# Performance work log

Measured on AMD Instinct MI355X. Metric: run time of the kernel, lower is better.

Reference implementation:

```python
import jax, jax.numpy as jnp
import numpy as np

B, S, D = 4, 2048, 1024

def setup_inputs() -> dict:
    key = jax.random.key(0)
    k1, k2, k3, k4 = jax.random.split(key, 4)
    scale = 1.0 / np.sqrt(D)
    x = jax.random.normal(k1, (B, S, D), dtype=jnp.float32)
    Wq = jax.random.normal(k2, (D, D), dtype=jnp.float32) * scale
    Wk = jax.random.normal(k3, (D, D), dtype=jnp.float32) * scale
    Wv = jax.random.normal(k4, (D, D), dtype=jnp.float32) * scale
    return {"x": x, "Wq": Wq, "Wk": Wk, "Wv": Wv}

def reference(x, Wq, Wk, Wv):
    # Linear projections (nn.Linear with bias=False computes x @ W.T)
    q = jnp.einsum('bsd,ed->bse', x, Wq)
    k = jnp.einsum('bsd,ed->bse', x, Wk)
    v = jnp.einsum('bsd,ed->bse', x, Wv)
    # HRR binding: circular convolution of k and v == elementwise product in FFT domain
    fq = jnp.fft.fft(q, axis=-1)
    fk = jnp.fft.fft(k, axis=-1)
    fv = jnp.fft.fft(v, axis=-1)
    # Causal associative memory: cumulative sum of bound key-value pairs over sequence
    mem = jnp.cumsum(fk * fv, axis=-2)  # [B, S, D] complex
    # Unbind with query via approximate inverse (complex conjugate of fft(q))
    out = jnp.fft.ifft(mem * jnp.conj(fq), axis=-1).real
    return out.astype(x.dtype)
```

## Files before the change

### kernel.cpp

```cpp
#include <hip/hip_runtime.h>

#define BB 4
#define SS 2048
#define DD 1024
#define MM 8192
#define CH 64
#define RR 32
#define PI_F 3.14159265358979323846f

typedef __attribute__((ext_vector_type(8))) short bf16x8;
typedef __attribute__((ext_vector_type(4))) float f32x4;

__device__ __forceinline__ unsigned short f2bf(float f) {
  unsigned int u = __float_as_uint(f);
  u = (u + 0x7FFFu + ((u >> 16) & 1u)) >> 16;
  return (unsigned short)u;
}
__device__ __forceinline__ float bf2f(unsigned short h) {
  return __uint_as_float(((unsigned int)h) << 16);
}

__global__ __launch_bounds__(256) void convert_bf16(
    const float* __restrict__ src, unsigned short* __restrict__ dst) {
  const long i = ((long)blockIdx.x * 256 + threadIdx.x) * 4;
  const float4 v = *(const float4*)&src[i];
  ushort4 o;
  o.x = f2bf(v.x); o.y = f2bf(v.y); o.z = f2bf(v.z); o.w = f2bf(v.w);
  *(ushort4*)&dst[i] = o;
}

__global__ __launch_bounds__(256) void convert_w(
    const float* __restrict__ Wq, const float* __restrict__ Wk,
    const float* __restrict__ Wv, unsigned short* __restrict__ dst) {
  const int z = blockIdx.y;
  const float* src = (z == 0) ? Wq : (z == 1) ? Wk : Wv;
  const long i = ((long)blockIdx.x * 256 + threadIdx.x) * 4;
  const float4 v = *(const float4*)&src[i];
  ushort4 o;
  o.x = f2bf(v.x); o.y = f2bf(v.y); o.z = f2bf(v.z); o.w = f2bf(v.w);
  *(ushort4*)&dst[(size_t)z * DD * DD + i] = o;
}

__device__ __forceinline__ void async16(const void* g, void* l) {
  __builtin_amdgcn_global_load_lds(
      (const __attribute__((address_space(1))) void*)g,
      (__attribute__((address_space(3))) void*)l, 16, 0, 0);
}

__global__ __launch_bounds__(256) void gemm_mfma(
    const unsigned short* __restrict__ xb,
    const unsigned short* __restrict__ Wb,
    float* __restrict__ outq, unsigned short* __restrict__ KV) {
  const int z = blockIdx.z;
  const unsigned short* W = Wb + (size_t)z * DD * DD;

  __shared__ unsigned short Als[128 * 64];
  __shared__ unsigned short Bls[128 * 64];

  const int tid  = threadIdx.x;
  const int lane = tid & 63;
  const int wave = tid >> 6;
  const int wm = (wave & 1) * 64;
  const int wn = (wave >> 1) * 64;

  const long m0 = (long)blockIdx.x * 128;
  const long n0 = (long)blockIdx.y * 128;

  f32x4 acc[4][4] = {};

  for (int k0 = 0; k0 < DD; k0 += 64) {
    #pragma unroll
    for (int i = 0; i < 4; ++i) {
      const int slot = i * 256 + tid;
      const int row  = slot >> 3;
      const int kq   = slot & 7;
      const int g    = kq ^ (row & 7);
      async16(xb + (m0 + row) * DD + k0 + g * 8, &Als[slot * 8]);
      async16(W  + (n0 + row) * DD + k0 + g * 8, &Bls[slot * 8]);
    }
    __syncthreads();

    const int fr = lane & 15;
    const int kq = lane >> 4;
    #pragma unroll
    for (int h = 0; h < 2; ++h) {
      bf16x8 af[4], bfr[4];
      #pragma unroll
      for (int mt = 0; mt < 4; ++mt) {
        const int row = wm + mt * 16 + fr;
        af[mt] = *(const bf16x8*)
            &Als[row * 64 + ((((h << 2) + kq) ^ (fr & 7)) << 3)];
      }
      #pragma unroll
      for (int nt = 0; nt < 4; ++nt) {
        const int row = wn + nt * 16 + fr;
        bfr[nt] = *(const bf16x8*)
            &Bls[row * 64 + ((((h << 2) + kq) ^ (fr & 7)) << 3)];
      }
      #pragma unroll
      for (int mt = 0; mt < 4; ++mt)
        #pragma unroll
        for (int nt = 0; nt < 4; ++nt)
          acc[mt][nt] = __builtin_amdgcn_mfma_f32_16x16x32_bf16(
              af[mt], bfr[nt], acc[mt][nt], 0, 0, 0);
    }
    __syncthreads();
  }

  const int col = lane & 15;
  const int r0  = (lane >> 4) * 4;
  if (z == 0) {
    #pragma unroll
    for (int mt = 0; mt < 4; ++mt)
      #pragma unroll
      for (int nt = 0; nt < 4; ++nt)
        #pragma unroll
        for (int r = 0; r < 4; ++r) {
          const long m = m0 + wm + mt * 16 + r0 + r;
          const long n = n0 + wn + nt * 16 + col;
          outq[m * DD + n] = acc[mt][nt][r];
        }
  } else {
    unsigned short* Ck = KV + (size_t)(z - 1) * DD;
    #pragma unroll
    for (int mt = 0; mt < 4; ++mt)
      #pragma unroll
      for (int nt = 0; nt < 4; ++nt)
        #pragma unroll
        for (int r = 0; r < 4; ++r) {
          const long m = m0 + wm + mt * 16 + r0 + r;
          const long n = n0 + wn + nt * 16 + col;
          Ck[m * 2048 + n] = f2bf(acc[mt][nt][r]);
        }
  }
}

__device__ __forceinline__ int pidx(int i) { return i + (i >> 6); }
#define BUFSZ 1040
__device__ __forceinline__ int pidx16(int i) { return i + (i >> 4); }
#define MEMSZ 546

__device__ __forceinline__ int rev4(int p) {
  unsigned r = __brev((unsigned)p) >> 22;
  return (int)(((r & 0x155u) << 1) | ((r & 0x2AAu) >> 1));
}

__host__ __device__ constexpr int clog2(int s) {
  return (s == 256) ? 8 : (s == 64) ? 6 : (s == 16) ? 4 : (s == 4) ? 2 : 0;
}

template <int S>
__device__ __forceinline__ void fwd_stage(float2 x[4], int t) {
  float c1 = 1.0f, s1 = 0.0f;
  if (S > 1) {
    const int j = t & (S - 1);
    __sincosf(-2.0f * PI_F * (float)j / (float)(4 * S), &s1, &c1);
  }
  const float c2 = c1 * c1 - s1 * s1, s2 = 2.0f * c1 * s1;
  const float c3 = c1 * c2 - s1 * s2, s3 = c1 * s2 + s1 * c2;
  const float Ar = x[0].x + x[2].x, Ai = x[0].y + x[2].y;
  const float Br = x[1].x + x[3].x, Bi = x[1].y + x[3].y;
  const float Cr = x[0].x - x[2].x, Ci = x[0].y - x[2].y;
  const float dr = x[1].x - x[3].x, di = x[1].y - x[3].y;
  const float y1r = Cr + di, y1i = Ci - dr;
  const float y2r = Ar - Br, y2i = Ai - Bi;
  const float y3r = Cr - di, y3i = Ci + dr;
  x[0] = make_float2(Ar + Br, Ai + Bi);
  x[1] = make_float2(y1r * c1 - y1i * s1, y1r * s1 + y1i * c1);
  x[2] = make_float2(y2r * c2 - y2i * s2, y2r * s2 + y2i * c2);
  x[3] = make_float2(y3r * c3 - y3i * s3, y3r * s3 + y3i * c3);
}

template <int S>
__device__ __forceinline__ void inv_stage(float2 x[4], int t) {
  float c1 = 1.0f, s1 = 0.0f;
  if (S > 1) {
    const int j = t & (S - 1);
    __sincosf(2.0f * PI_F * (float)j / (float)(4 * S), &s1, &c1);
  }
  const float c2 = c1 * c1 - s1 * s1, s2 = 2.0f * c1 * s1;
  const float c3 = c1 * c2 - s1 * s2, s3 = c1 * s2 + s1 * c2;
  const float u0r = x[0].x,                   u0i = x[0].y;
  const float u1r = x[1].x * c1 - x[1].y * s1, u1i = x[1].x * s1 + x[1].y * c1;
  const float u2r = x[2].x * c2 - x[2].y * s2, u2i = x[2].x * s2 + x[2].y * c2;
  const float u3r = x[3].x * c3 - x[3].y * s3, u3i = x[3].x * s3 + x[3].y * c3;
  const float Er = u0r + u2r, Ei = u0i + u2i;
  const float Fr = u0r - u2r, Fi = u0i - u2i;
  const float Gr = u1r + u3r, Gi = u1i + u3i;
  const float Hr = u1r - u3r, Hi = u1i - u3i;
  x[0] = make_float2(Er + Gr, Ei + Gi);
  x[1] = make_float2(Fr - Hi, Fi + Hr);
  x[2] = make_float2(Er - Gr, Ei - Gi);
  x[3] = make_float2(Fr + Hi, Fi - Hr);
}

template <int SW, int SR>
__device__ __forceinline__ void xchg(float2* buf, float2 x[4], int t) {
  constexpr int LW = clog2(SW), LR = clog2(SR);
  #pragma unroll
  for (int n = 0; n < 4; ++n)
    buf[pidx(((t >> LW) << (LW + 2)) + (t & (SW - 1)) + n * SW)] = x[n];
  __syncthreads();
  #pragma unroll
  for (int n = 0; n < 4; ++n)
    x[n] = buf[pidx(((t >> LR) << (LR + 2)) + (t & (SR - 1)) + n * SR)];
  __syncthreads();
}

__device__ __forceinline__ void fwd_fft(float2* buf, float2 x[4], int t) {
  fwd_stage<256>(x, t); xchg<256, 64>(buf, x, t);
  fwd_stage<64>(x, t);  xchg<64, 16>(buf, x, t);
  fwd_stage<16>(x, t);  xchg<16, 4>(buf, x, t);
  fwd_stage<4>(x, t);   xchg<4, 1>(buf, x, t);
  fwd_stage<1>(x, t);
  #pragma unroll
  for (int n = 0; n < 4; ++n) buf[pidx(4 * t + n)] = x[n];
  __syncthreads();
}

__global__ __launch_bounds__(256) void bind_kernel(unsigned short* __restrict__ KV) {
  __shared__ float2 buf[BUFSZ];
  const int t = threadIdx.x;
  unsigned short* row = KV + (long)blockIdx.x * 2048;

  float2 x[4];
  #pragma unroll
  for (int n = 0; n < 4; ++n) {
    const int i = t + 256 * n;
    x[n] = make_float2(bf2f(row[i]), bf2f(row[1024 + i]));
  }
  fwd_fft(buf, x, t);

  float2* Prow = (float2*)row;
  #pragma unroll
  for (int m = 0; m < 2; ++m) {
    const int s = t + 256 * m;
    if (s == 0) {
      const float2 W0   = buf[pidx(0)];
      const float2 W512 = buf[pidx(2)];
      Prow[0] = make_float2(W0.x * W0.y, W512.x * W512.y);
    } else {
      const int p1 = rev4(s);
      const int p2 = rev4(1024 - s);
      const float2 F1 = buf[pidx(p1)], F2 = buf[pidx(p2)];
      const float fkr = 0.5f * (F1.x + F2.x), fki = 0.5f * (F1.y - F2.y);
      const float fvr = 0.5f * (F1.y + F2.y), fvi = 0.5f * (F2.x - F1.x);
      Prow[s] = make_float2(fkr * fvr - fki * fvi, fkr * fvi + fki * fvr);
    }
  }
}

__global__ __launch_bounds__(256) void scan_chunk_sum(
    const float2* __restrict__ P, float2* __restrict__ csum) {
  const int chunk = blockIdx.x;
  const int batch = blockIdx.y >> 1;
  const int f = (blockIdx.y & 1) * 256 + threadIdx.x;
  long base = ((long)batch * SS + (long)chunk * RR) * 512 + f;
  float sr = 0.0f, si = 0.0f;
  #pragma unroll 4
  for (int i = 0; i < RR; ++i) {
    float2 p = P[base + (long)i * 512];
    sr += p.x; si += p.y;
  }
  csum[((long)batch * CH + chunk) * 512 + f] = make_float2(sr, si);
}

__global__ __launch_bounds__(256) void scan_chunk_scan(float2* csum) {
  const int idx = blockIdx.x * 256 + threadIdx.x;
  const int batch = idx >> 9;
  const int f = idx & 511;
  float2 v[CH];
  #pragma unroll
  for (int c = 0; c < CH; ++c) v[c] = csum[((long)batch * CH + c) * 512 + f];
  float rr = 0.0f, ri = 0.0f;
  #pragma unroll
  for (int c = 0; c < CH; ++c) {
    const float2 x = v[c];
    csum[((long)batch * CH + c) * 512 + f] = make_float2(rr, ri);
    rr += x.x; ri += x.y;
  }
}

__global__ __launch_bounds__(256) void scan_apply(
    float2* __restrict__ P, const float2* __restrict__ csum) {
  const int chunk = blockIdx.x;
  const int batch = blockIdx.y >> 1;
  const int f = (blockIdx.y & 1) * 256 + threadIdx.x;
  float2 off = csum[((long)batch * CH + chunk) * 512 + f];
  float ar = off.x, ai = off.y;
  long base = ((long)batch * SS + (long)chunk * RR) * 512 + f;
  for (int i = 0; i < RR; ++i) {
    const long o = base + (long)i * 512;
    float2 p = P[o];
    ar += p.x; ai += p.y;
    P[o] = make_float2(ar, ai);
  }
}

__global__ __launch_bounds__(256) void unbind_kernel(
    float* __restrict__ qout, const float2* __restrict__ mem) {
  __shared__ float2 buf[BUFSZ];
  __shared__ float2 m0s[MEMSZ], m1s[MEMSZ];
  const int t = threadIdx.x;
  const long r0 = (long)blockIdx.x * 2;
  float* row0 = qout + r0 * DD;
  float* row1 = row0 + DD;
  const float2* mem0 = mem + r0 * 512;
  const float2* mem1 = mem0 + 512;

  float2 x[4];
  #pragma unroll
  for (int n = 0; n < 4; ++n) {
    const int i = t + 256 * n;
    x[n] = make_float2(row0[i], row1[i]);
  }
  #pragma unroll
  for (int n = 0; n < 2; ++n) {
    const int s = t + 256 * n;
    const float2 a = mem0[s], b = mem1[s];
    if (s == 0) {
      m0s[pidx16(0)]   = make_float2(a.x, 0.0f);
      m0s[pidx16(512)] = make_float2(a.y, 0.0f);
      m1s[pidx16(0)]   = make_float2(b.x, 0.0f);
      m1s[pidx16(512)] = make_float2(b.y, 0.0f);
    } else {
      m0s[pidx16(s)] = a;
      m1s[pidx16(s)] = b;
    }
  }
  fwd_fft(buf, x, t);

  float2 z[4];
  #pragma unroll
  for (int m = 0; m < 4; ++m) {
    const int p   = t + 256 * m;
    const int bin = rev4(p);
    const int p2  = rev4((1024 - bin) & 1023);
    const float2 F1 = buf[pidx(p)], F2 = buf[pidx(p2)];
    const float q0r = 0.5f * (F1.x + F2.x), q0i = 0.5f * (F1.y - F2.y);
    const float q1r = 0.5f * (F1.y + F2.y), q1i = 0.5f * (F2.x - F1.x);
    const int  ix = (bin <= 512) ? bin : 1024 - bin;
    const float sg = (bin <= 512) ? 1.0f : -1.0f;
    float2 m0 = m0s[pidx16(ix)], m1 = m1s[pidx16(ix)];
    m0.y *= sg; m1.y *= sg;
    const float z0r = m0.x * q0r + m0.y * q0i, z0i = m0.y * q0r - m0.x * q0i;
    const float z1r = m1.x * q1r + m1.y * q1i, z1i = m1.y * q1r - m1.x * q1i;
    z[m] = make_float2(z0r - z1i, z0i + z1r);
  }
  __syncthreads();
  #pragma unroll
  for (int m = 0; m < 4; ++m) buf[pidx(t + 256 * m)] = z[m];
  __syncthreads();
  #pragma unroll
  for (int n = 0; n < 4; ++n) x[n] = buf[pidx(4 * t + n)];

  inv_stage<1>(x, t);   xchg<1, 4>(buf, x, t);
  inv_stage<4>(x, t);   xchg<4, 16>(buf, x, t);
  inv_stage<16>(x, t);  xchg<16, 64>(buf, x, t);
  inv_stage<64>(x, t);  xchg<64, 256>(buf, x, t);
  inv_stage<256>(x, t);

  const float sc = 1.0f / 1024.0f;
  #pragma unroll
  for (int n = 0; n < 4; ++n) {
    const int i = t + 256 * n;
    row0[i] = x[n].x * sc;
    row1[i] = x[n].y * sc;
  }
}

extern "C" void kernel_launch(void* const* d_in, const int* in_sizes, int n_in,
                              void* d_out, int out_size, void* d_ws, size_t ws_size,
                              hipStream_t stream) {
  (void)in_sizes; (void)n_in; (void)out_size;
  const float* x  = (const float*)d_in[0];
  const float* Wq = (const float*)d_in[1];
  const float* Wk = (const float*)d_in[2];
  const float* Wv = (const float*)d_in[3];
  float* out = (float*)d_out;

  const size_t wbytes = (size_t)3 * DD * DD * 2;
  auto need = [&](size_t MHr, size_t nB) {
    return wbytes + MHr * DD * 2 + MHr * 4096 + nB * CH * 512 * 8;
  };
  const int nPass = (ws_size >= need(8192, 4)) ? 1 : 2;
  const size_t MH = MM / nPass;
  const int    nB = BB / nPass;

  char* ws = (char*)d_ws;
  unsigned short* Wb = (unsigned short*)ws;
  unsigned short* xb = (unsigned short*)(ws + wbytes);
  unsigned short* KV = (unsigned short*)(ws + wbytes + MH * DD * 2);
  float2*       csum = (float2*)((char*)KV + MH * 4096);

  convert_w<<<dim3(DD * DD / 1024, 3), 256, 0, stream>>>(Wq, Wk, Wv, Wb);

  for (int h = 0; h < nPass; ++h) {
    const float* xh   = x   + (size_t)h * MH * DD;
    float*       outh = out + (size_t)h * MH * DD;

    convert_bf16<<<MH * DD / 1024, 256, 0, stream>>>(xh, xb);
    gemm_mfma<<<dim3(MH / 128, DD / 128, 3), 256, 0, stream>>>(xb, Wb, outh, KV);
    bind_kernel<<<MH, 256, 0, stream>>>(KV);
    scan_chunk_sum<<<dim3(CH, nB * 2), 256, 0, stream>>>((const float2*)KV, csum);
    scan_chunk_scan<<<nB * 2, 256, 0, stream>>>(csum);
    scan_apply<<<dim3(CH, nB * 2), 256, 0, stream>>>((float2*)KV, csum);
    unbind_kernel<<<MH / 2, 256, 0, stream>>>(outh, (const float2*)KV);
  }
}
```

Before: 234.2 us.

## Run FFTs per wavefront without block barriers, interleave K/V, merge conversions

Each bind/unbind FFT now runs on a single 64-lane wavefront holding 16 elements per lane, with per-wave LDS buffers. This replaces the __syncthreads barriers with compiler fences and turns the first and last stage exchanges into register transposes. The GEMM writes K and V interleaved so bind can read both with one 32-bit load. Unbind reads the memory spectrum straight from global instead of staging it in LDS, and the weight and x conversions are merged into one launch. In exchange the kernels use more registers per thread and four times the LDS per block, and correctness relies on intra-wave lockstep for the LDS exchanges.

```diff
diff --git a/kernel.cpp b/kernel.cpp
--- a/kernel.cpp
+++ b/kernel.cpp
@@ -11,6 +11,8 @@
 typedef __attribute__((ext_vector_type(8))) short bf16x8;
 typedef __attribute__((ext_vector_type(4))) float f32x4;
 
+#define DSFENCE asm volatile("" ::: "memory")
+
 __device__ __forceinline__ unsigned short f2bf(float f) {
   unsigned int u = __float_as_uint(f);
   u = (u + 0x7FFFu + ((u >> 16) & 1u)) >> 16;
@@ -20,25 +22,28 @@
   return __uint_as_float(((unsigned int)h) << 16);
 }
 
-__global__ __launch_bounds__(256) void convert_bf16(
-    const float* __restrict__ src, unsigned short* __restrict__ dst) {
-  const long i = ((long)blockIdx.x * 256 + threadIdx.x) * 4;
+__global__ __launch_bounds__(256) void convert_all(
+    const float* __restrict__ xs, const float* __restrict__ Wq,
+    const float* __restrict__ Wk, const float* __restrict__ Wv,
+    unsigned short* __restrict__ xb, unsigned short* __restrict__ Wb, int nx) {
+  const int b = blockIdx.x;
+  const float* src;
+  unsigned short* dst;
+  long off;
+  if (b < nx) {
+    src = xs; dst = xb; off = (long)b * 1024;
+  } else {
+    const int wb = b - nx;
+    const int z = wb >> 10;
+    src = (z == 0) ? Wq : (z == 1) ? Wk : Wv;
+    dst = Wb + (size_t)z * DD * DD;
+    off = (long)(wb & 1023) * 1024;
+  }
+  const long i = off + (long)threadIdx.x * 4;
   const float4 v = *(const float4*)&src[i];
   ushort4 o;
   o.x = f2bf(v.x); o.y = f2bf(v.y); o.z = f2bf(v.z); o.w = f2bf(v.w);
   *(ushort4*)&dst[i] = o;
-}
-
-__global__ __launch_bounds__(256) void convert_w(
-    const float* __restrict__ Wq, const float* __restrict__ Wk,
-    const float* __restrict__ Wv, unsigned short* __restrict__ dst) {
-  const int z = blockIdx.y;
-  const float* src = (z == 0) ? Wq : (z == 1) ? Wk : Wv;
-  const long i = ((long)blockIdx.x * 256 + threadIdx.x) * 4;
-  const float4 v = *(const float4*)&src[i];
-  ushort4 o;
-  o.x = f2bf(v.x); o.y = f2bf(v.y); o.z = f2bf(v.z); o.w = f2bf(v.w);
-  *(ushort4*)&dst[(size_t)z * DD * DD + i] = o;
 }
 
 __device__ __forceinline__ void async16(const void* g, void* l) {
@@ -121,7 +126,7 @@
           outq[m * DD + n] = acc[mt][nt][r];
         }
   } else {
-    unsigned short* Ck = KV + (size_t)(z - 1) * DD;
+    unsigned short* Ck = KV + (z - 1);
     #pragma unroll
     for (int mt = 0; mt < 4; ++mt)
       #pragma unroll
@@ -130,15 +135,13 @@
         for (int r = 0; r < 4; ++r) {
           const long m = m0 + wm + mt * 16 + r0 + r;
           const long n = n0 + wn + nt * 16 + col;
-          Ck[m * 2048 + n] = f2bf(acc[mt][nt][r]);
+          Ck[m * 2048 + 2 * n] = f2bf(acc[mt][nt][r]);
         }
   }
 }
 
 __device__ __forceinline__ int pidx(int i) { return i + (i >> 6); }
 #define BUFSZ 1040
-__device__ __forceinline__ int pidx16(int i) { return i + (i >> 4); }
-#define MEMSZ 546
 
 __device__ __forceinline__ int rev4(int p) {
   unsigned r = __brev((unsigned)p) >> 22;
@@ -194,55 +197,90 @@
   x[3] = make_float2(Fr + Hi, Fi - Hr);
 }
 
+__device__ __forceinline__ void xpose(float2 x[4][4]) {
+  #pragma unroll
+  for (int a = 0; a < 4; ++a)
+    #pragma unroll
+    for (int b = a + 1; b < 4; ++b) {
+      const float2 tmp = x[a][b]; x[a][b] = x[b][a]; x[b][a] = tmp;
+    }
+}
+
 template <int SW, int SR>
-__device__ __forceinline__ void xchg(float2* buf, float2 x[4], int t) {
+__device__ __forceinline__ void xchg_w(float2* wbuf, float2 x[4][4], int l) {
   constexpr int LW = clog2(SW), LR = clog2(SR);
   #pragma unroll
-  for (int n = 0; n < 4; ++n)
-    buf[pidx(((t >> LW) << (LW + 2)) + (t & (SW - 1)) + n * SW)] = x[n];
-  __syncthreads();
-  #pragma unroll
-  for (int n = 0; n < 4; ++n)
-    x[n] = buf[pidx(((t >> LR) << (LR + 2)) + (t & (SR - 1)) + n * SR)];
-  __syncthreads();
-}
-
-__device__ __forceinline__ void fwd_fft(float2* buf, float2 x[4], int t) {
-  fwd_stage<256>(x, t); xchg<256, 64>(buf, x, t);
-  fwd_stage<64>(x, t);  xchg<64, 16>(buf, x, t);
-  fwd_stage<16>(x, t);  xchg<16, 4>(buf, x, t);
-  fwd_stage<4>(x, t);   xchg<4, 1>(buf, x, t);
-  fwd_stage<1>(x, t);
-  #pragma unroll
-  for (int n = 0; n < 4; ++n) buf[pidx(4 * t + n)] = x[n];
-  __syncthreads();
+  for (int j = 0; j < 4; ++j) {
+    const int t = l + 64 * j;
+    #pragma unroll
+    for (int n = 0; n < 4; ++n)
+      wbuf[pidx(((t >> LW) << (LW + 2)) + (t & (SW - 1)) + n * SW)] = x[j][n];
+  }
+  DSFENCE;
+  #pragma unroll
+  for (int j = 0; j < 4; ++j) {
+    const int t = l + 64 * j;
+    #pragma unroll
+    for (int n = 0; n < 4; ++n)
+      x[j][n] = wbuf[pidx(((t >> LR) << (LR + 2)) + (t & (SR - 1)) + n * SR)];
+  }
+  DSFENCE;
+}
+
+__device__ __forceinline__ void fwd_fft_wave(float2* wbuf, float2 x[4][4], int l) {
+  #pragma unroll
+  for (int j = 0; j < 4; ++j) fwd_stage<256>(x[j], l + 64 * j);
+  xpose(x);
+  #pragma unroll
+  for (int j = 0; j < 4; ++j) fwd_stage<64>(x[j], l + 64 * j);
+  xchg_w<64, 16>(wbuf, x, l);
+  #pragma unroll
+  for (int j = 0; j < 4; ++j) fwd_stage<16>(x[j], l + 64 * j);
+  xchg_w<16, 4>(wbuf, x, l);
+  #pragma unroll
+  for (int j = 0; j < 4; ++j) fwd_stage<4>(x[j], l + 64 * j);
+  xchg_w<4, 1>(wbuf, x, l);
+  #pragma unroll
+  for (int j = 0; j < 4; ++j) fwd_stage<1>(x[j], l + 64 * j);
+  #pragma unroll
+  for (int j = 0; j < 4; ++j)
+    #pragma unroll
+    for (int n = 0; n < 4; ++n)
+      wbuf[pidx(4 * (l + 64 * j) + n)] = x[j][n];
+  DSFENCE;
 }
 
 __global__ __launch_bounds__(256) void bind_kernel(unsigned short* __restrict__ KV) {
-  __shared__ float2 buf[BUFSZ];
-  const int t = threadIdx.x;
-  unsigned short* row = KV + (long)blockIdx.x * 2048;
-
-  float2 x[4];
-  #pragma unroll
-  for (int n = 0; n < 4; ++n) {
-    const int i = t + 256 * n;
-    x[n] = make_float2(bf2f(row[i]), bf2f(row[1024 + i]));
-  }
-  fwd_fft(buf, x, t);
-
-  float2* Prow = (float2*)row;
-  #pragma unroll
-  for (int m = 0; m < 2; ++m) {
-    const int s = t + 256 * m;
+  __shared__ float2 sbuf[4][BUFSZ];
+  const int l = threadIdx.x & 63;
+  const int w = threadIdx.x >> 6;
+  float2* wbuf = sbuf[w];
+  unsigned short* rp = KV + ((long)blockIdx.x * 4 + w) * 2048;
+  const unsigned int* rp32 = (const unsigned int*)rp;
+
+  float2 x[4][4];
+  #pragma unroll
+  for (int j = 0; j < 4; ++j)
+    #pragma unroll
+    for (int n = 0; n < 4; ++n) {
+      const unsigned int u = rp32[l + 64 * j + 256 * n];
+      x[j][n] = make_float2(bf2f((unsigned short)(u & 0xffffu)),
+                            bf2f((unsigned short)(u >> 16)));
+    }
+  fwd_fft_wave(wbuf, x, l);
+
+  float2* Prow = (float2*)rp;
+  #pragma unroll
+  for (int u = 0; u < 8; ++u) {
+    const int s = l + 64 * u;
     if (s == 0) {
-      const float2 W0   = buf[pidx(0)];
-      const float2 W512 = buf[pidx(2)];
+      const float2 W0   = wbuf[pidx(0)];
+      const float2 W512 = wbuf[pidx(2)];
       Prow[0] = make_float2(W0.x * W0.y, W512.x * W512.y);
     } else {
       const int p1 = rev4(s);
       const int p2 = rev4(1024 - s);
-      const float2 F1 = buf[pidx(p1)], F2 = buf[pidx(p2)];
+      const float2 F1 = wbuf[pidx(p1)], F2 = wbuf[pidx(p2)];
       const float fkr = 0.5f * (F1.x + F2.x), fki = 0.5f * (F1.y - F2.y);
       const float fvr = 0.5f * (F1.y + F2.y), fvi = 0.5f * (F2.x - F1.x);
       Prow[s] = make_float2(fkr * fvr - fki * fvi, fkr * fvi + fki * fvr);
@@ -299,74 +337,90 @@
 
 __global__ __launch_bounds__(256) void unbind_kernel(
     float* __restrict__ qout, const float2* __restrict__ mem) {
-  __shared__ float2 buf[BUFSZ];
-  __shared__ float2 m0s[MEMSZ], m1s[MEMSZ];
-  const int t = threadIdx.x;
-  const long r0 = (long)blockIdx.x * 2;
+  __shared__ float2 sbuf[4][BUFSZ];
+  const int l = threadIdx.x & 63;
+  const int w = threadIdx.x >> 6;
+  float2* wbuf = sbuf[w];
+  const long r0 = ((long)blockIdx.x * 4 + w) * 2;
   float* row0 = qout + r0 * DD;
   float* row1 = row0 + DD;
   const float2* mem0 = mem + r0 * 512;
   const float2* mem1 = mem0 + 512;
 
-  float2 x[4];
-  #pragma unroll
-  for (int n = 0; n < 4; ++n) {
-    const int i = t + 256 * n;
-    x[n] = make_float2(row0[i], row1[i]);
-  }
-  #pragma unroll
-  for (int n = 0; n < 2; ++n) {
-    const int s = t + 256 * n;
-    const float2 a = mem0[s], b = mem1[s];
-    if (s == 0) {
-      m0s[pidx16(0)]   = make_float2(a.x, 0.0f);
-      m0s[pidx16(512)] = make_float2(a.y, 0.0f);
-      m1s[pidx16(0)]   = make_float2(b.x, 0.0f);
-      m1s[pidx16(512)] = make_float2(b.y, 0.0f);
-    } else {
-      m0s[pidx16(s)] = a;
-      m1s[pidx16(s)] = b;
-    }
-  }
-  fwd_fft(buf, x, t);
-
-  float2 z[4];
-  #pragma unroll
-  for (int m = 0; m < 4; ++m) {
-    const int p   = t + 256 * m;
-    const int bin = rev4(p);
-    const int p2  = rev4((1024 - bin) & 1023);
-    const float2 F1 = buf[pidx(p)], F2 = buf[pidx(p2)];
-    const float q0r = 0.5f * (F1.x + F2.x), q0i = 0.5f * (F1.y - F2.y);
-    const float q1r = 0.5f * (F1.y + F2.y), q1i = 0.5f * (F2.x - F1.x);
-    const int  ix = (bin <= 512) ? bin : 1024 - bin;
-    const float sg = (bin <= 512) ? 1.0f : -1.0f;
-    float2 m0 = m0s[pidx16(ix)], m1 = m1s[pidx16(ix)];
-    m0.y *= sg; m1.y *= sg;
-    const float z0r = m0.x * q0r + m0.y * q0i, z0i = m0.y * q0r - m0.x * q0i;
-    const float z1r = m1.x * q1r + m1.y * q1i, z1i = m1.y * q1r - m1.x * q1i;
-    z[m] = make_float2(z0r - z1i, z0i + z1r);
-  }
-  __syncthreads();
-  #pragma unroll
-  for (int m = 0; m < 4; ++m) buf[pidx(t + 256 * m)] = z[m];
-  __syncthreads();
-  #pragma unroll
-  for (int n = 0; n < 4; ++n) x[n] = buf[pidx(4 * t + n)];
-
-  inv_stage<1>(x, t);   xchg<1, 4>(buf, x, t);
-  inv_stage<4>(x, t);   xchg<4, 16>(buf, x, t);
-  inv_stage<16>(x, t);  xchg<16, 64>(buf, x, t);
-  inv_stage<64>(x, t);  xchg<64, 256>(buf, x, t);
-  inv_stage<256>(x, t);
+  float2 x[4][4];
+  #pragma unroll
+  for (int j = 0; j < 4; ++j)
+    #pragma unroll
+    for (int n = 0; n < 4; ++n) {
+      const int i = l + 64 * j + 256 * n;
+      x[j][n] = make_float2(row0[i], row1[i]);
+    }
+  fwd_fft_wave(wbuf, x, l);
+
+  float2 z[4][4];
+  #pragma unroll
+  for (int j = 0; j < 4; ++j)
+    #pragma unroll
+    for (int m = 0; m < 4; ++m) {
+      const int p   = l + 64 * j + 256 * m;
+      const int bin = rev4(p);
+      const int p2  = rev4((1024 - bin) & 1023);
+      const float2 F1 = wbuf[pidx(p)], F2 = wbuf[pidx(p2)];
+      const float q0r = 0.5f * (F1.x + F2.x), q0i = 0.5f * (F1.y - F2.y);
+      const float q1r = 0.5f * (F1.y + F2.y), q1i = 0.5f * (F2.x - F1.x);
+      float2 m0, m1;
+      if (bin == 0 || bin == 512) {
+        const float2 a = mem0[0], b = mem1[0];
+        m0 = make_float2(bin ? a.y : a.x, 0.0f);
+        m1 = make_float2(bin ? b.y : b.x, 0.0f);
+      } else {
+        const int  ix = (bin < 512) ? bin : 1024 - bin;
+        const float sg = (bin < 512) ? 1.0f : -1.0f;
+        m0 = mem0[ix]; m1 = mem1[ix];
+        m0.y *= sg; m1.y *= sg;
+      }
+      const float z0r = m0.x * q0r + m0.y * q0i, z0i = m0.y * q0r - m0.x * q0i;
+      const float z1r = m1.x * q1r + m1.y * q1i, z1i = m1.y * q1r - m1.x * q1i;
+      z[j][m] = make_float2(z0r - z1i, z0i + z1r);
+    }
+  DSFENCE;
+  #pragma unroll
+  for (int j = 0; j < 4; ++j)
+    #pragma unroll
+    for (int m = 0; m < 4; ++m)
+      wbuf[pidx(l + 64 * j + 256 * m)] = z[j][m];
+  DSFENCE;
+  #pragma unroll
+  for (int j = 0; j < 4; ++j)
+    #pragma unroll
+    for (int n = 0; n < 4; ++n)
+      x[j][n] = wbuf[pidx(4 * (l + 64 * j) + n)];
+  DSFENCE;
+
+  #pragma unroll
+  for (int j = 0; j < 4; ++j) inv_stage<1>(x[j], l + 64 * j);
+  xchg_w<1, 4>(wbuf, x, l);
+  #pragma unroll
+  for (int j = 0; j < 4; ++j) inv_stage<4>(x[j], l + 64 * j);
+  xchg_w<4, 16>(wbuf, x, l);
+  #pragma unroll
+  for (int j = 0; j < 4; ++j) inv_stage<16>(x[j], l + 64 * j);
+  xchg_w<16, 64>(wbuf, x, l);
+  #pragma unroll
+  for (int j = 0; j < 4; ++j) inv_stage<64>(x[j], l + 64 * j);
+  xpose(x);
+  #pragma unroll
+  for (int j = 0; j < 4; ++j) inv_stage<256>(x[j], l + 64 * j);
 
   const float sc = 1.0f / 1024.0f;
   #pragma unroll
-  for (int n = 0; n < 4; ++n) {
-    const int i = t + 256 * n;
-    row0[i] = x[n].x * sc;
-    row1[i] = x[n].y * sc;
-  }
+  for (int j = 0; j < 4; ++j)
+    #pragma unroll
+    for (int n = 0; n < 4; ++n) {
+      const int i = l + 64 * j + 256 * n;
+      row0[i] = x[j][n].x * sc;
+      row1[i] = x[j][n].y * sc;
+    }
 }
 
 extern "C" void kernel_launch(void* const* d_in, const int* in_sizes, int n_in,
@@ -393,18 +447,18 @@
   unsigned short* KV = (unsigned short*)(ws + wbytes + MH * DD * 2);
   float2*       csum = (float2*)((char*)KV + MH * 4096);
 
-  convert_w<<<dim3(DD * DD / 1024, 3), 256, 0, stream>>>(Wq, Wk, Wv, Wb);
-
+  const int nx = (int)(MH * DD / 1024);
   for (int h = 0; h < nPass; ++h) {
     const float* xh   = x   + (size_t)h * MH * DD;
     float*       outh = out + (size_t)h * MH * DD;
 
-    convert_bf16<<<MH * DD / 1024, 256, 0, stream>>>(xh, xb);
+    convert_all<<<nx + (h == 0 ? 3072 : 0), 256, 0, stream>>>(
+        xh, Wq, Wk, Wv, xb, Wb, nx);
     gemm_mfma<<<dim3(MH / 128, DD / 128, 3), 256, 0, stream>>>(xb, Wb, outh, KV);
-    bind_kernel<<<MH, 256, 0, stream>>>(KV);
+    bind_kernel<<<MH / 4, 256, 0, stream>>>(KV);
     scan_chunk_sum<<<dim3(CH, nB * 2), 256, 0, stream>>>((const float2*)KV, csum);
     scan_chunk_scan<<<nB * 2, 256, 0, stream>>>(csum);
     scan_apply<<<dim3(CH, nB * 2), 256, 0, stream>>>((float2*)KV, csum);
-    unbind_kernel<<<MH / 2, 256, 0, stream>>>(outh, (const float2*)KV);
-  }
-}
+    unbind_kernel<<<MH / 8, 256, 0, stream>>>(outh, (const float2*)KV);
+  }
+}
```

Result: slower. 241.0 us (+2.9%).
